# Performance work log

Measured on AMD Instinct MI355X. Metric: run time of the kernel, lower is better.

## Reference

```python
import jax, jax.numpy as jnp
import numpy as np

K = 3
PAD = 1

def conv2d(x, w, b, pad):
    out = jax.lax.conv_general_dilated(
        x, w, window_strides=(1, 1), padding=[(pad, pad), (pad, pad)],
        dimension_numbers=("NCHW", "OIHW", "NCHW"))
    return out + b[None, :, None, None]

def bilinear_sample(x, ys, xs):
    # x: [B,C,H,W]; ys,xs: [B,K2,H,W] fractional sample coords (zero outside)
    B, C, H, W = x.shape
    y0f = jnp.floor(ys); x0f = jnp.floor(xs)
    iy0 = y0f.astype(jnp.int32); ix0 = x0f.astype(jnp.int32)
    iy1 = iy0 + 1; ix1 = ix0 + 1
    wy1 = ys - y0f; wy0 = 1.0 - wy1
    wx1 = xs - x0f; wx0 = 1.0 - wx1
    b_idx = jnp.arange(B)[:, None, None, None]
    def fetch(iy, ix):
        valid = (iy >= 0) & (iy < H) & (ix >= 0) & (ix < W)
        iyc = jnp.clip(iy, 0, H - 1)
        ixc = jnp.clip(ix, 0, W - 1)
        v = x[b_idx, :, iyc, ixc]  # [B,K2,H,W,C]
        return v * valid[..., None].astype(x.dtype)
    return (fetch(iy0, ix0) * (wy0 * wx0)[..., None]
          + fetch(iy0, ix1) * (wy0 * wx1)[..., None]
          + fetch(iy1, ix0) * (wy1 * wx0)[..., None]
          + fetch(iy1, ix1) * (wy1 * wx1)[..., None])

def setup_inputs() -> dict:
    key = jax.random.key(0)
    k1, k2, k3, k4, k5 = jax.random.split(key, 5)
    B, C, H, W = 8, 128, 64, 64
    O = 128
    K2 = K * K
    x = jax.random.normal(k1, (B, C, H, W), dtype=jnp.float32)
    # offset-predicting conv: small init so sample offsets stay O(1)
    offset_w = jax.random.normal(k2, (2 * K2, C, K, K), dtype=jnp.float32) * 0.01
    offset_b = jax.random.normal(k3, (2 * K2,), dtype=jnp.float32) * 0.01
    # deformable conv weight/bias, fan-in scaled
    weight = jax.random.normal(k4, (O, C, K, K), dtype=jnp.float32) / np.sqrt(C * K2)
    bias = jax.random.normal(k5, (O,), dtype=jnp.float32) * 0.01
    return {"x": x, "offset_w": offset_w, "offset_b": offset_b,
            "weight": weight, "bias": bias}

def reference(x, offset_w, offset_b, weight, bias):
    B, C, H, W = x.shape
    K2 = K * K
    # standard conv predicting 2*K2 offsets per output pixel
    offsets = conv2d(x, offset_w, offset_b, PAD)             # [B,2*K2,H,W]
    off = offsets.reshape(B, K2, 2, H, W)                    # (dy,dx) per tap
    dy = off[:, :, 0]; dx = off[:, :, 1]                     # [B,K2,H,W]
    kk = jnp.arange(K, dtype=jnp.float32)
    kh = jnp.repeat(kk, K)                                    # [K2] row-major
    kw = jnp.tile(kk, K)
    # sampling locations: p0 - pad + p_k + offset
    ys = (jnp.arange(H, dtype=jnp.float32) - PAD)[None, None, :, None] \
         + kh[None, :, None, None] + dy
    xs = (jnp.arange(W, dtype=jnp.float32) - PAD)[None, None, None, :] \
         + kw[None, :, None, None] + dx
    sampled = bilinear_sample(x, ys, xs)                     # [B,K2,H,W,C]
    w = weight.reshape(weight.shape[0], C, K2)               # [O,C,K2]
    out = jnp.einsum("bkhwc,ock->bohw", sampled, w)
    return out + bias[None, :, None, None]
```

## Files before the change

kernel.cpp:

```cpp
#include <hip/hip_runtime.h>
#include <stdint.h>

constexpr int B = 8, C = 128, H = 64, W = 64, O = 128;
constexpr int HW = H * W;

typedef __bf16 bf16x8 __attribute__((ext_vector_type(8)));
typedef float f32x4 __attribute__((ext_vector_type(4)));
typedef float f32x16 __attribute__((ext_vector_type(16)));
typedef unsigned int ux4 __attribute__((ext_vector_type(4)));

static __device__ __forceinline__ unsigned pack_pair(__bf16 a, __bf16 b) {
    unsigned short ua = __builtin_bit_cast(unsigned short, a);
    unsigned short ub = __builtin_bit_cast(unsigned short, b);
    return (unsigned)ua | ((unsigned)ub << 16);
}

__global__ void wsplit_kernel(const float* __restrict__ w,
                              __bf16* __restrict__ wBhi, __bf16* __restrict__ wBlo) {
    int idx = blockIdx.x * 256 + threadIdx.x;
    int kk = idx & 31;
    int o = (idx >> 5) & 127;
    int chunk = idx >> 12;
    int tap = chunk >> 2, ch = chunk & 3;
    int c = ch * 32 + kk;
    float v = w[(o * C + c) * 9 + tap];
    __bf16 h = (__bf16)v;
    int seg = kk >> 3, e = kk & 7;
    int dst = chunk * 4096 + (o >> 5) * 1024 + (seg >> 1) * 512 + (seg & 1) * 256 + (o & 31) * 8 + e;
    wBhi[dst] = h;
    wBlo[dst] = (__bf16)(v - (float)h);
}

__global__ void otrans_kernel(const float* __restrict__ ow, float* __restrict__ owT) {
    int idx = blockIdx.x * 256 + threadIdx.x;
    if (idx >= C * 9 * 18) return;
    int oc = idx % 18;
    int tap = (idx / 18) % 9;
    int c = idx / (18 * 9);
    owT[(c * 9 + tap) * 20 + oc] = ow[(oc * C + c) * 9 + tap];
}

__global__ __launch_bounds__(256) void xtrans_kernel(const float* __restrict__ x,
                                                     float* __restrict__ xt) {
    __shared__ float tile[64][133];
    int t = threadIdx.x;
    int bid = blockIdx.x;
    int b = bid >> 6, y = bid & 63;
    int px = t & 63, cseg = t >> 6;
    const float* xp = x + (size_t)(b * C + cseg * 32) * HW + y * W + px;
#pragma unroll
    for (int i = 0; i < 32; ++i)
        tile[px][cseg * 32 + i] = xp[(size_t)i * HW];
    __syncthreads();
    float* dst = xt + ((size_t)b * HW + y * W) * 128;
#pragma unroll
    for (int j = 0; j < 8; ++j) {
        int flat = j * 1024 + t * 4;
        int ppx = flat >> 7, c = flat & 127;
        f32x4 v;
        v[0] = tile[ppx][c + 0];
        v[1] = tile[ppx][c + 1];
        v[2] = tile[ppx][c + 2];
        v[3] = tile[ppx][c + 3];
        *(f32x4*)&dst[flat] = v;
    }
}

__global__ __launch_bounds__(256) void offconv_part_kernel(
    const float* __restrict__ x, const float* __restrict__ owT,
    float* __restrict__ part) {
    __shared__ float ws[32 * 9 * 20];
    __shared__ float s_red[4][18][64];
    int t = threadIdx.x;
    int bid = blockIdx.x;
    int swz = (bid & 7) * 256 + (bid >> 3);
    int cg = swz & 3;
    int y = (swz >> 2) & 63;
    int b = swz >> 8;
    int px = t & 63, sub = t >> 6;
    const float* src = owT + cg * 5760;
    for (int i = t; i < 5760; i += 256) ws[i] = src[i];
    float m[9];
    int aoff[9];
#pragma unroll
    for (int kh = 0; kh < 3; ++kh)
#pragma unroll
        for (int kw = 0; kw < 3; ++kw) {
            int yy = y + kh - 1, xx = px + kw - 1;
            bool v = (yy >= 0 && yy < H && xx >= 0 && xx < W);
            m[kh * 3 + kw] = v ? 1.f : 0.f;
            aoff[kh * 3 + kw] = min(max(yy, 0), H - 1) * W + min(max(xx, 0), W - 1);
        }
    __syncthreads();
    float acc[18];
#pragma unroll
    for (int o = 0; o < 18; ++o) acc[o] = 0.f;
    const float* xcg = x + (b * C + cg * 32 + sub * 8) * HW;
    for (int c8 = 0; c8 < 8; ++c8) {
        const float* xp = xcg + c8 * HW;
        float xv[9];
#pragma unroll
        for (int tp = 0; tp < 9; ++tp) xv[tp] = m[tp] * xp[aoff[tp]];
        const float* wp = ws + (sub * 8 + c8) * 180;
#pragma unroll
        for (int tp = 0; tp < 9; ++tp) {
            float v = xv[tp];
            float4 w0 = *(const float4*)&wp[tp * 20 + 0];
            float4 w1 = *(const float4*)&wp[tp * 20 + 4];
            float4 w2 = *(const float4*)&wp[tp * 20 + 8];
            float4 w3 = *(const float4*)&wp[tp * 20 + 12];
            float2 w4 = *(const float2*)&wp[tp * 20 + 16];
            acc[0] += v * w0.x;  acc[1] += v * w0.y;  acc[2] += v * w0.z;  acc[3] += v * w0.w;
            acc[4] += v * w1.x;  acc[5] += v * w1.y;  acc[6] += v * w1.z;  acc[7] += v * w1.w;
            acc[8] += v * w2.x;  acc[9] += v * w2.y;  acc[10] += v * w2.z; acc[11] += v * w2.w;
            acc[12] += v * w3.x; acc[13] += v * w3.y; acc[14] += v * w3.z; acc[15] += v * w3.w;
            acc[16] += v * w4.x; acc[17] += v * w4.y;
        }
    }
#pragma unroll
    for (int o = 0; o < 18; ++o) s_red[sub][o][px] = acc[o];
    __syncthreads();
    for (int flat = t; flat < 18 * 64; flat += 256) {
        int oc = flat >> 6, p = flat & 63;
        float v = s_red[0][oc][p] + s_red[1][oc][p] + s_red[2][oc][p] + s_red[3][oc][p];
        part[(cg * B + b) * 18 * HW + oc * HW + y * 64 + p] = v;
    }
}

__global__ void offreduce_kernel(const float* __restrict__ part,
                                 const float* __restrict__ ob,
                                 float* __restrict__ offs) {
    int idx = blockIdx.x * 256 + threadIdx.x;
    int oc = (idx >> 12) % 18;
    constexpr int S = B * 18 * HW;
    offs[idx] = ob[oc] + part[idx] + part[S + idx] + part[2 * S + idx] + part[3 * S + idx];
}

struct BiLin { float w00, w01, w10, w11; int a00, a01, a10, a11; };
static __device__ __forceinline__ BiLin bilin_calc(const float* __restrict__ offs,
                                                   int b, int tap, int y, int px) {
    BiLin r;
    int kh = tap / 3, kw = tap % 3;
    float dy = offs[(b * 18 + 2 * tap) * HW + y * 64 + px];
    float dx = offs[(b * 18 + 2 * tap + 1) * HW + y * 64 + px];
    float ys = (float)(y - 1 + kh) + dy;
    float xs = (float)(px - 1 + kw) + dx;
    float yf = floorf(ys), xf = floorf(xs);
    int iy0 = (int)yf, ix0 = (int)xf;
    int iy1 = iy0 + 1, ix1 = ix0 + 1;
    float wy1 = ys - yf, wy0 = 1.f - wy1;
    float wx1 = xs - xf, wx0 = 1.f - wx1;
    bool vy0 = (iy0 >= 0) & (iy0 < H), vy1 = (iy1 >= 0) & (iy1 < H);
    bool vx0 = (ix0 >= 0) & (ix0 < W), vx1 = (ix1 >= 0) & (ix1 < W);
    int iy0c = min(max(iy0, 0), H - 1), iy1c = min(max(iy1, 0), H - 1);
    int ix0c = min(max(ix0, 0), W - 1), ix1c = min(max(ix1, 0), W - 1);
    r.w00 = (vy0 && vx0) ? wy0 * wx0 : 0.f;
    r.w01 = (vy0 && vx1) ? wy0 * wx1 : 0.f;
    r.w10 = (vy1 && vx0) ? wy1 * wx0 : 0.f;
    r.w11 = (vy1 && vx1) ? wy1 * wx1 : 0.f;
    r.a00 = iy0c * W + ix0c;
    r.a01 = iy0c * W + ix1c;
    r.a10 = iy1c * W + ix0c;
    r.a11 = iy1c * W + ix1c;
    return r;
}

__global__ __launch_bounds__(256, 4) void deform_fused_kernel(
    const float* __restrict__ xt, const float* __restrict__ offs,
    const __bf16* __restrict__ wBhi, const __bf16* __restrict__ wBlo,
    const float* __restrict__ bias, float* __restrict__ out) {
    __shared__ uint2 Ah[2][256], Al[2][256];
    int t = threadIdx.x;
    int bid = blockIdx.x;
    int swz = (bid & 7) * 128 + (bid >> 3);
    int b = swz >> 7;
    int y = (swz >> 1) & 63;
    int half = swz & 1;
    int px0 = half * 32;
    int row0 = y * W;
    const float* xb = xt + (size_t)b * HW * 128;
    int l31 = t & 31, lhi = (t >> 5) & 1, wv = t >> 6;
    int o = wv * 32 + l31;
    int spx = t & 31;
    int g = t >> 5;

    BiLin s{};
    f32x4 gq0, gq1, gq2, gq3;
    auto issueA = [&](int chunk) {
        int tap = chunk >> 2, ch = chunk & 3;
        if ((chunk & 3) == 0) s = bilin_calc(offs, b, tap, y, px0 + spx);
        int c0 = ch * 32 + g * 4;
        const float* base = xb + c0;
        gq0 = *(const f32x4*)(base + (size_t)s.a00 * 128);
        gq1 = *(const f32x4*)(base + (size_t)s.a01 * 128);
        gq2 = *(const f32x4*)(base + (size_t)s.a10 * 128);
        gq3 = *(const f32x4*)(base + (size_t)s.a11 * 128);
    };
    auto finishA = [&](int bi) {
        float v[4];
#pragma unroll
        for (int c = 0; c < 4; ++c)
            v[c] = s.w00 * gq0[c] + s.w01 * gq1[c] + s.w10 * gq2[c] + s.w11 * gq3[c];
        __bf16 h0 = (__bf16)v[0], h1 = (__bf16)v[1], h2 = (__bf16)v[2], h3 = (__bf16)v[3];
        uint2 qh, ql;
        qh.x = pack_pair(h0, h1);
        qh.y = pack_pair(h2, h3);
        ql.x = pack_pair((__bf16)(v[0] - (float)h0), (__bf16)(v[1] - (float)h1));
        ql.y = pack_pair((__bf16)(v[2] - (float)h2), (__bf16)(v[3] - (float)h3));
        int idx = (g >> 1) * 64 + spx * 2 + (g & 1);
        Ah[bi][idx] = qh;
        Al[bi][idx] = ql;
    };
    ux4 bhc[2], blc[2], bhn[2], bln[2];
    auto issueB = [&](int chunk, ux4* bh, ux4* bl) {
        size_t fo = (size_t)chunk * 4096 + wv * 1024 + lhi * 256 + l31 * 8;
        const __bf16* ph = wBhi + fo;
        const __bf16* pl = wBlo + fo;
        bh[0] = *(const ux4*)(ph);
        bh[1] = *(const ux4*)(ph + 512);
        bl[0] = *(const ux4*)(pl);
        bl[1] = *(const ux4*)(pl + 512);
    };
    f32x16 acc;
    {
        float bv = bias[o];
#pragma unroll
        for (int j = 0; j < 16; ++j) acc[j] = bv;
    }
    issueB(0, bhc, blc);
    issueA(0);
    finishA(0);
    __syncthreads();
#pragma unroll 1
    for (int i = 0; i < 36; ++i) {
        int bi = i & 1;
        if (i < 35) {
            issueB(i + 1, bhn, bln);
            issueA(i + 1);
        }
#pragma unroll
        for (int sI = 0; sI < 2; ++sI) {
            int u = sI * 2 + lhi;
            bf16x8 ah = __builtin_bit_cast(bf16x8, *(const ux4*)&Ah[bi][u * 64 + l31 * 2]);
            bf16x8 al = __builtin_bit_cast(bf16x8, *(const ux4*)&Al[bi][u * 64 + l31 * 2]);
            bf16x8 bh = __builtin_bit_cast(bf16x8, bhc[sI]);
            bf16x8 bl = __builtin_bit_cast(bf16x8, blc[sI]);
            acc = __builtin_amdgcn_mfma_f32_32x32x16_bf16(ah, bh, acc, 0, 0, 0);
            acc = __builtin_amdgcn_mfma_f32_32x32x16_bf16(al, bh, acc, 0, 0, 0);
            acc = __builtin_amdgcn_mfma_f32_32x32x16_bf16(ah, bl, acc, 0, 0, 0);
        }
        if (i < 35) finishA(bi ^ 1);
        __syncthreads();
        bhc[0] = bhn[0]; bhc[1] = bhn[1];
        blc[0] = bln[0]; blc[1] = bln[1];
    }
    float* op = out + ((size_t)b * O + o) * HW + row0 + px0;
#pragma unroll
    for (int gq = 0; gq < 4; ++gq) {
        f32x4 v4;
        v4[0] = acc[gq * 4 + 0];
        v4[1] = acc[gq * 4 + 1];
        v4[2] = acc[gq * 4 + 2];
        v4[3] = acc[gq * 4 + 3];
        *(f32x4*)(op + gq * 8 + lhi * 4) = v4;
    }
}

extern "C" void kernel_launch(void* const* d_in, const int* in_sizes, int n_in,
                              void* d_out, int out_size, void* d_ws, size_t ws_size,
                              hipStream_t stream) {
    const float* x        = (const float*)d_in[0];
    const float* offset_w = (const float*)d_in[1];
    const float* offset_b = (const float*)d_in[2];
    const float* weight   = (const float*)d_in[3];
    const float* bias     = (const float*)d_in[4];
    float* out = (float*)d_out;

    float* offs = (float*)d_ws;
    float* part = offs + B * 18 * HW;
    float* owT  = part + 4 * B * 18 * HW;
    __bf16* wBhi = (__bf16*)(owT + 128 * 9 * 20);
    __bf16* wBlo = wBhi + 36 * 128 * 32;
    float* xt   = (float*)(wBlo + 36 * 128 * 32);

    wsplit_kernel<<<576, 256, 0, stream>>>(weight, wBhi, wBlo);
    otrans_kernel<<<(C * 9 * 18 + 255) / 256, 256, 0, stream>>>(offset_w, owT);
    xtrans_kernel<<<B * H, 256, 0, stream>>>(x, xt);
    offconv_part_kernel<<<2048, 256, 0, stream>>>(x, owT, part);
    offreduce_kernel<<<(B * 18 * HW) / 256, 256, 0, stream>>>(part, offset_b, offs);
    deform_fused_kernel<<<1024, 256, 0, stream>>>(xt, offs, wBhi, wBlo, bias, out);
}
```

Measured before the change: 208.1 us.

## Widen deform block to full row and stage weights through LDS

Each block now handles a full 64-pixel output row with 8 waves arranged as 2 pixel halves by 4 output groups. bf16 hi/lo weight tiles are loaded cooperatively into double-buffered shared memory instead of per-wave register loads. The bilinear gather is issued two chunks ahead so its latency overlaps the MFMA work. This cuts redundant global weight traffic but increases LDS use and halves the grid size, which may reduce occupancy.

```diff
diff --git a/kernel.cpp b/kernel.cpp
--- a/kernel.cpp
+++ b/kernel.cpp
@@ -165,96 +165,112 @@
     return r;
 }
 
-__global__ __launch_bounds__(256, 4) void deform_fused_kernel(
+__global__ __launch_bounds__(512, 4) void deform_fused_kernel(
     const float* __restrict__ xt, const float* __restrict__ offs,
     const __bf16* __restrict__ wBhi, const __bf16* __restrict__ wBlo,
     const float* __restrict__ bias, float* __restrict__ out) {
-    __shared__ uint2 Ah[2][256], Al[2][256];
+    __shared__ uint2 AhL[2][512], AlL[2][512];
+    __shared__ __bf16 BldsH[2][4096], BldsL[2][4096];
+
     int t = threadIdx.x;
     int bid = blockIdx.x;
-    int swz = (bid & 7) * 128 + (bid >> 3);
-    int b = swz >> 7;
-    int y = (swz >> 1) & 63;
-    int half = swz & 1;
-    int px0 = half * 32;
+    int swz = (bid & 7) * 64 + (bid >> 3);
+    int b = swz >> 6, y = swz & 63;
     int row0 = y * W;
     const float* xb = xt + (size_t)b * HW * 128;
-    int l31 = t & 31, lhi = (t >> 5) & 1, wv = t >> 6;
-    int o = wv * 32 + l31;
-    int spx = t & 31;
-    int g = t >> 5;
+
+    int lane = t & 63;
+    int wv = t >> 6;
+    int l31 = t & 31, lhi = (t >> 5) & 1;
+    int wm = wv & 1, wn = wv >> 1;
+    int o = wn * 32 + l31;
+
+    int ppx = (wv & 3) * 16 + (lane >> 2);
+    int q = lane & 3;
+    int chalf = wv >> 2;
+    int g = chalf * 4 + q;
 
     BiLin s{};
-    f32x4 gq0, gq1, gq2, gq3;
-    auto issueA = [&](int chunk) {
+    f32x4 greg[4];
+    auto issueG = [&](int chunk) {
         int tap = chunk >> 2, ch = chunk & 3;
-        if ((chunk & 3) == 0) s = bilin_calc(offs, b, tap, y, px0 + spx);
-        int c0 = ch * 32 + g * 4;
-        const float* base = xb + c0;
-        gq0 = *(const f32x4*)(base + (size_t)s.a00 * 128);
-        gq1 = *(const f32x4*)(base + (size_t)s.a01 * 128);
-        gq2 = *(const f32x4*)(base + (size_t)s.a10 * 128);
-        gq3 = *(const f32x4*)(base + (size_t)s.a11 * 128);
-    };
-    auto finishA = [&](int bi) {
-        float v[4];
-#pragma unroll
-        for (int c = 0; c < 4; ++c)
-            v[c] = s.w00 * gq0[c] + s.w01 * gq1[c] + s.w10 * gq2[c] + s.w11 * gq3[c];
-        __bf16 h0 = (__bf16)v[0], h1 = (__bf16)v[1], h2 = (__bf16)v[2], h3 = (__bf16)v[3];
+        if ((chunk & 3) == 0) s = bilin_calc(offs, b, tap, y, ppx);
+        const float* base = xb + ch * 32 + chalf * 16 + q * 4;
+        greg[0] = *(const f32x4*)(base + (size_t)s.a00 * 128);
+        greg[1] = *(const f32x4*)(base + (size_t)s.a01 * 128);
+        greg[2] = *(const f32x4*)(base + (size_t)s.a10 * 128);
+        greg[3] = *(const f32x4*)(base + (size_t)s.a11 * 128);
+    };
+    auto finishA = [&](int bufi) {
+        float v0 = s.w00 * greg[0][0] + s.w01 * greg[1][0] + s.w10 * greg[2][0] + s.w11 * greg[3][0];
+        float v1 = s.w00 * greg[0][1] + s.w01 * greg[1][1] + s.w10 * greg[2][1] + s.w11 * greg[3][1];
+        float v2 = s.w00 * greg[0][2] + s.w01 * greg[1][2] + s.w10 * greg[2][2] + s.w11 * greg[3][2];
+        float v3 = s.w00 * greg[0][3] + s.w01 * greg[1][3] + s.w10 * greg[2][3] + s.w11 * greg[3][3];
+        __bf16 h0 = (__bf16)v0, h1 = (__bf16)v1, h2 = (__bf16)v2, h3 = (__bf16)v3;
         uint2 qh, ql;
         qh.x = pack_pair(h0, h1);
         qh.y = pack_pair(h2, h3);
-        ql.x = pack_pair((__bf16)(v[0] - (float)h0), (__bf16)(v[1] - (float)h1));
-        ql.y = pack_pair((__bf16)(v[2] - (float)h2), (__bf16)(v[3] - (float)h3));
-        int idx = (g >> 1) * 64 + spx * 2 + (g & 1);
-        Ah[bi][idx] = qh;
-        Al[bi][idx] = ql;
-    };
-    ux4 bhc[2], blc[2], bhn[2], bln[2];
-    auto issueB = [&](int chunk, ux4* bh, ux4* bl) {
-        size_t fo = (size_t)chunk * 4096 + wv * 1024 + lhi * 256 + l31 * 8;
-        const __bf16* ph = wBhi + fo;
-        const __bf16* pl = wBlo + fo;
-        bh[0] = *(const ux4*)(ph);
-        bh[1] = *(const ux4*)(ph + 512);
-        bl[0] = *(const ux4*)(pl);
-        bl[1] = *(const ux4*)(pl + 512);
-    };
+        ql.x = pack_pair((__bf16)(v0 - (float)h0), (__bf16)(v1 - (float)h1));
+        ql.y = pack_pair((__bf16)(v2 - (float)h2), (__bf16)(v3 - (float)h3));
+        int idx = (g >> 1) * 128 + ppx * 2 + (g & 1);
+        AhL[bufi][idx] = qh;
+        AlL[bufi][idx] = ql;
+    };
+
+    ux4 bregH, bregL;
+    auto issueBload = [&](int chunk) {
+        const __bf16* ph = wBhi + (size_t)chunk * 4096 + wv * 512 + lane * 8;
+        const __bf16* pl = wBlo + (size_t)chunk * 4096 + wv * 512 + lane * 8;
+        bregH = *(const ux4*)ph;
+        bregL = *(const ux4*)pl;
+    };
+    auto writeB = [&](int bufi) {
+        *(ux4*)&BldsH[bufi][wv * 512 + lane * 8] = bregH;
+        *(ux4*)&BldsL[bufi][wv * 512 + lane * 8] = bregL;
+    };
+
     f32x16 acc;
     {
         float bv = bias[o];
 #pragma unroll
         for (int j = 0; j < 16; ++j) acc[j] = bv;
     }
-    issueB(0, bhc, blc);
-    issueA(0);
-    finishA(0);
-    __syncthreads();
-#pragma unroll 1
-    for (int i = 0; i < 36; ++i) {
-        int bi = i & 1;
-        if (i < 35) {
-            issueB(i + 1, bhn, bln);
-            issueA(i + 1);
-        }
+
+    auto domfma = [&](int bufi) {
 #pragma unroll
         for (int sI = 0; sI < 2; ++sI) {
             int u = sI * 2 + lhi;
-            bf16x8 ah = __builtin_bit_cast(bf16x8, *(const ux4*)&Ah[bi][u * 64 + l31 * 2]);
-            bf16x8 al = __builtin_bit_cast(bf16x8, *(const ux4*)&Al[bi][u * 64 + l31 * 2]);
-            bf16x8 bh = __builtin_bit_cast(bf16x8, bhc[sI]);
-            bf16x8 bl = __builtin_bit_cast(bf16x8, blc[sI]);
+            bf16x8 ah = __builtin_bit_cast(bf16x8, *(const ux4*)&AhL[bufi][u * 128 + (wm * 32 + l31) * 2]);
+            bf16x8 al = __builtin_bit_cast(bf16x8, *(const ux4*)&AlL[bufi][u * 128 + (wm * 32 + l31) * 2]);
+            bf16x8 bh = __builtin_bit_cast(bf16x8, *(const ux4*)&BldsH[bufi][wn * 1024 + sI * 512 + lhi * 256 + l31 * 8]);
+            bf16x8 bl = __builtin_bit_cast(bf16x8, *(const ux4*)&BldsL[bufi][wn * 1024 + sI * 512 + lhi * 256 + l31 * 8]);
             acc = __builtin_amdgcn_mfma_f32_32x32x16_bf16(ah, bh, acc, 0, 0, 0);
             acc = __builtin_amdgcn_mfma_f32_32x32x16_bf16(al, bh, acc, 0, 0, 0);
             acc = __builtin_amdgcn_mfma_f32_32x32x16_bf16(ah, bl, acc, 0, 0, 0);
         }
-        if (i < 35) finishA(bi ^ 1);
+    };
+
+    issueG(0);
+    issueBload(0);
+    finishA(0);
+    writeB(0);
+    issueG(1);
+    __syncthreads();
+
+#pragma unroll 1
+    for (int i = 0; i < 36; ++i) {
+        int bi = i & 1;
+        if (i < 35) issueBload(i + 1);
+        domfma(bi);
+        if (i < 35) {
+            finishA(bi ^ 1);
+            writeB(bi ^ 1);
+        }
         __syncthreads();
-        bhc[0] = bhn[0]; bhc[1] = bhn[1];
-        blc[0] = bln[0]; blc[1] = bln[1];
-    }
-    float* op = out + ((size_t)b * O + o) * HW + row0 + px0;
+        if (i < 34) issueG(i + 2);
+    }
+
+    float* op = out + ((size_t)b * O + o) * HW + row0 + wm * 32;
 #pragma unroll
     for (int gq = 0; gq < 4; ++gq) {
         f32x4 v4;
@@ -288,5 +304,5 @@
     xtrans_kernel<<<B * H, 256, 0, stream>>>(x, xt);
     offconv_part_kernel<<<2048, 256, 0, stream>>>(x, owT, part);
     offreduce_kernel<<<(B * 18 * HW) / 256, 256, 0, stream>>>(part, offset_b, offs);
-    deform_fused_kernel<<<1024, 256, 0, stream>>>(xt, offs, wBhi, wBlo, bias, out);
-}
+    deform_fused_kernel<<<512, 512, 0, stream>>>(xt, offs, wBhi, wBlo, bias, out);
+}
```

Result: faster. 174.7 us (-16.0%).
